# Kernel tuning notes

Measured on AMD Instinct MI355X. Metric: run time of the kernel, lower is better.

The kernel has to match this reference:

```python
import jax, jax.numpy as jnp
import numpy as np

B, T, I, H = 64, 2048, 64, 128


def setup_inputs() -> dict:
    key = jax.random.key(0)
    ks = jax.random.split(key, 6)
    std = 1.0 / np.sqrt(H)
    return {
        "x": jax.random.normal(ks[0], (B, T, I), dtype=jnp.float32),
        "h0": jax.random.normal(ks[1], (B, H), dtype=jnp.float32),
        "W": jax.random.uniform(ks[2], (H, I), dtype=jnp.float32, minval=-std, maxval=std),
        "U": jax.random.uniform(ks[3], (H, H), dtype=jnp.float32, minval=-std, maxval=std),
        "b_ih": jax.random.uniform(ks[4], (H,), dtype=jnp.float32, minval=-std, maxval=std),
        "b_hh": jax.random.uniform(ks[5], (H,), dtype=jnp.float32, minval=-std, maxval=std),
    }


def reference(x, h0, W, U, b_ih, b_hh):
    # Precompute the input projection for all timesteps in one big GEMM:
    # xw[b,t,h] = W x_t + b_ih + b_hh  (biases folded in once)
    xw = jnp.einsum("bti,hi->bth", x, W) + b_ih + b_hh  # [B,T,H]
    xw_t = jnp.swapaxes(xw, 0, 1)  # [T,B,H] for scan over time

    def step(h, xt):
        # vanilla tanh RNN cell: h' = tanh(W x + U h + b_ih + b_hh)
        h_new = jnp.tanh(xt + h @ U.T)
        return h_new, h_new

    h_last, ys = jax.lax.scan(step, h0, xw_t)  # ys: [T,B,H]
    output = jnp.swapaxes(ys, 0, 1)  # batch_first -> [B,T,H]
    return output, h_last
```

## Files before the change

kernel.cpp:

```cpp
#include <hip/hip_runtime.h>
#include <hip/hip_bf16.h>


#define RNN_B 64
#define RNN_T 2048
#define RNN_I 64
#define RNN_H 128
#define CH    32
#define NCH   (RNN_T / CH)

__device__ __forceinline__ float fast_tanh(float x) {
  float e = __builtin_amdgcn_exp2f(x * 2.885390081777927f);
  return 1.0f - 2.0f * __builtin_amdgcn_rcpf(e + 1.0f);
}

template <int CTRL>
__device__ __forceinline__ float dpp_add(float s) {
  int o = __builtin_amdgcn_mov_dpp(__float_as_int(s), CTRL, 0xF, 0xF, true);
  return s + __int_as_float(o);
}

__global__ __launch_bounds__(256) void rnn_xw_gemm(
    const float* __restrict__ x, const float* __restrict__ W,
    const float* __restrict__ b_ih, const float* __restrict__ b_hh,
    float* __restrict__ xw) {
  const int tid  = threadIdx.x;
  const int h    = tid >> 1;
  const int half = tid & 1;

  const float4* W4 = (const float4*)(W + h * RNN_I + half * 32);
  float4 w[8];
#pragma unroll
  for (int j = 0; j < 8; ++j) w[j] = W4[j];
  const float bias = b_ih[h] + b_hh[h];

  __shared__ __align__(16) float4 xs[64 * 16];
  const long rbase = (long)blockIdx.x * 64;
  const float4* xg = (const float4*)(x + rbase * RNN_I);
#pragma unroll
  for (int j = 0; j < 4; ++j) xs[tid + 256 * j] = xg[tid + 256 * j];
  __syncthreads();

  for (int r = 0; r < 64; ++r) {
    const float4* xr = xs + r * 16 + half * 8;
    float4 a = make_float4(0.f, 0.f, 0.f, 0.f);
#pragma unroll
    for (int j = 0; j < 8; ++j) {
      float4 xv = xr[j];
      a.x = fmaf(w[j].x, xv.x, a.x);
      a.y = fmaf(w[j].y, xv.y, a.y);
      a.z = fmaf(w[j].z, xv.z, a.z);
      a.w = fmaf(w[j].w, xv.w, a.w);
    }
    float s = (a.x + a.y) + (a.z + a.w);
    s = dpp_add<0xB1>(s);
    if (half == 0)
      xw[(rbase + r) * RNN_H + h] = s + bias;
  }
}

__global__ __launch_bounds__(512, 2) void rnn_scan(
    const float* xw,
    float* out, float* __restrict__ hlast,
    const float* __restrict__ h0, const float* __restrict__ U) {
  const int b   = blockIdx.x;
  const int tid = threadIdx.x;
  const int h   = tid >> 2;
  const int q   = tid & 3;

  __shared__ __align__(16) float hbuf[2][4 * 36];
  __shared__ __align__(16) float xbuf[CH * RNN_H];
  __shared__ __align__(16) float obuf[CH * RNN_H];

  const float4* U4 = (const float4*)(U + h * RNN_H + q * 32);
  float4 u[8];
#pragma unroll
  for (int j = 0; j < 8; ++j) u[j] = U4[j];

  if (tid < RNN_H) hbuf[0][(tid >> 5) * 36 + (tid & 31)] = h0[b * RNN_H + tid];

  const long base    = (long)b * RNN_T * RNN_H;
  const float4* xw4  = (const float4*)(xw + base);
  float4* out4       = (float4*)(out + base);
  float4* xb4        = (float4*)xbuf;
  const float4* ob4  = (const float4*)obuf;

  int cur = 0;
  for (int c = 0; c < NCH; ++c) {
    float4 xr0 = xw4[(long)c * 1024 + tid];
    float4 xr1 = xw4[(long)c * 1024 + tid + 512];
    if (c > 0) {
      float4 o0 = ob4[tid];
      float4 o1 = ob4[tid + 512];
      out4[(long)(c - 1) * 1024 + tid]       = o0;
      out4[(long)(c - 1) * 1024 + tid + 512] = o1;
    }
    xb4[tid]       = xr0;
    xb4[tid + 512] = xr1;
    __syncthreads();

    for (int tc = 0; tc < CH; ++tc) {
      const float4* hp = (const float4*)(hbuf[cur] + q * 36);
      float4 a = make_float4(0.f, 0.f, 0.f, 0.f);
#pragma unroll
      for (int j = 0; j < 8; ++j) {
        float4 hv = hp[j];
        a.x = fmaf(u[j].x, hv.x, a.x);
        a.y = fmaf(u[j].y, hv.y, a.y);
        a.z = fmaf(u[j].z, hv.z, a.z);
        a.w = fmaf(u[j].w, hv.w, a.w);
      }
      float s = (a.x + a.y) + (a.z + a.w);
      s = dpp_add<0xB1>(s);
      s = dpp_add<0x4E>(s);
      float val = fast_tanh(s + xbuf[tc * RNN_H + h]);
      if (q == 0) hbuf[cur ^ 1][(h >> 5) * 36 + (h & 31)] = val;
      if (q == 1) obuf[tc * RNN_H + h] = val;
      cur ^= 1;
      __syncthreads();
    }
  }

  out4[(long)(NCH - 1) * 1024 + tid]       = ob4[tid];
  out4[(long)(NCH - 1) * 1024 + tid + 512] = ob4[tid + 512];
  if (tid < RNN_H)
    hlast[b * RNN_H + tid] = hbuf[cur][(tid >> 5) * 36 + (tid & 31)];
}

extern "C" void kernel_launch(void* const* d_in, const int* in_sizes, int n_in,
                              void* d_out, int out_size, void* d_ws, size_t ws_size,
                              hipStream_t stream) {
  const float* x    = (const float*)d_in[0];
  const float* h0   = (const float*)d_in[1];
  const float* W    = (const float*)d_in[2];
  const float* U    = (const float*)d_in[3];
  const float* b_ih = (const float*)d_in[4];
  const float* b_hh = (const float*)d_in[5];

  float* out   = (float*)d_out;
  float* hlast = out + (long)RNN_B * RNN_T * RNN_H;

  rnn_xw_gemm<<<(RNN_B * RNN_T) / 64, 256, 0, stream>>>(x, W, b_ih, b_hh, out);
  rnn_scan<<<RNN_B, 512, 0, stream>>>(out, out, hlast, h0, U);
}
```

Before: 770.5 us.

## Register-tile input GEMM over shared W and force inline-asm FMAs in scan

The input-projection GEMM drops the per-thread W-in-registers layout with DPP reduction. It now stages both the x tile and all of W in padded shared memory, and each thread computes a 4x8 register tile of outputs, which raises reuse and removes the cross-lane reduction. The recurrent scan's inner dot product is rewritten with four independent accumulators issued via inline-asm v_fma_f32 after loading all h values up front. The asm is meant to stop the compiler reordering or contracting the FMAs, but it also hides them from scheduling. The scan dominates runtime and is latency-bound per step, so the GEMM change matters little overall.

```diff
diff --git a/kernel.cpp b/kernel.cpp
--- a/kernel.cpp
+++ b/kernel.cpp
@@ -20,42 +20,77 @@
   return s + __int_as_float(o);
 }
 
+#define FMA_V(acc, uu, hh) \
+  asm("v_fma_f32 %0, %1, %2, %0" : "+v"(acc) : "v"(uu), "v"(hh))
+
 __global__ __launch_bounds__(256) void rnn_xw_gemm(
     const float* __restrict__ x, const float* __restrict__ W,
     const float* __restrict__ b_ih, const float* __restrict__ b_hh,
     float* __restrict__ xw) {
-  const int tid  = threadIdx.x;
-  const int h    = tid >> 1;
-  const int half = tid & 1;
+  const int tid = threadIdx.x;
+  const int tr  = tid >> 4;
+  const int tc  = tid & 15;
 
-  const float4* W4 = (const float4*)(W + h * RNN_I + half * 32);
-  float4 w[8];
+  __shared__ __align__(16) float xs[64 * 68];
+  __shared__ __align__(16) float ws[128 * 68];
+
+  const long rbase = (long)blockIdx.x * 64;
+
+  {
+    const float4* xg = (const float4*)(x + rbase * RNN_I);
 #pragma unroll
-  for (int j = 0; j < 8; ++j) w[j] = W4[j];
-  const float bias = b_ih[h] + b_hh[h];
-
-  __shared__ __align__(16) float4 xs[64 * 16];
-  const long rbase = (long)blockIdx.x * 64;
-  const float4* xg = (const float4*)(x + rbase * RNN_I);
+    for (int j = 0; j < 4; ++j) {
+      int idx = tid + 256 * j;
+      int r = idx >> 4, k4 = idx & 15;
+      *(float4*)(&xs[r * 68 + k4 * 4]) = xg[idx];
+    }
+  }
+  {
+    const float4* wg = (const float4*)W;
 #pragma unroll
-  for (int j = 0; j < 4; ++j) xs[tid + 256 * j] = xg[tid + 256 * j];
+    for (int j = 0; j < 8; ++j) {
+      int idx = tid + 256 * j;
+      int c = idx >> 4, k4 = idx & 15;
+      *(float4*)(&ws[c * 68 + k4 * 4]) = wg[idx];
+    }
+  }
+  float bias[8];
+#pragma unroll
+  for (int cc = 0; cc < 8; ++cc)
+    bias[cc] = b_ih[tc + 16 * cc] + b_hh[tc + 16 * cc];
   __syncthreads();
 
-  for (int r = 0; r < 64; ++r) {
-    const float4* xr = xs + r * 16 + half * 8;
-    float4 a = make_float4(0.f, 0.f, 0.f, 0.f);
+  float acc[4][8];
 #pragma unroll
-    for (int j = 0; j < 8; ++j) {
-      float4 xv = xr[j];
-      a.x = fmaf(w[j].x, xv.x, a.x);
-      a.y = fmaf(w[j].y, xv.y, a.y);
-      a.z = fmaf(w[j].z, xv.z, a.z);
-      a.w = fmaf(w[j].w, xv.w, a.w);
-    }
-    float s = (a.x + a.y) + (a.z + a.w);
-    s = dpp_add<0xB1>(s);
-    if (half == 0)
-      xw[(rbase + r) * RNN_H + h] = s + bias;
+  for (int rr = 0; rr < 4; ++rr)
+#pragma unroll
+    for (int cc = 0; cc < 8; ++cc) acc[rr][cc] = 0.f;
+
+  for (int kc = 0; kc < 16; ++kc) {
+    float4 xv[4], wv[8];
+#pragma unroll
+    for (int rr = 0; rr < 4; ++rr)
+      xv[rr] = *(const float4*)(&xs[(tr + 16 * rr) * 68 + kc * 4]);
+#pragma unroll
+    for (int cc = 0; cc < 8; ++cc)
+      wv[cc] = *(const float4*)(&ws[(tc + 16 * cc) * 68 + kc * 4]);
+#pragma unroll
+    for (int rr = 0; rr < 4; ++rr)
+#pragma unroll
+      for (int cc = 0; cc < 8; ++cc) {
+        acc[rr][cc] = fmaf(xv[rr].x, wv[cc].x, acc[rr][cc]);
+        acc[rr][cc] = fmaf(xv[rr].y, wv[cc].y, acc[rr][cc]);
+        acc[rr][cc] = fmaf(xv[rr].z, wv[cc].z, acc[rr][cc]);
+        acc[rr][cc] = fmaf(xv[rr].w, wv[cc].w, acc[rr][cc]);
+      }
+  }
+
+#pragma unroll
+  for (int rr = 0; rr < 4; ++rr) {
+    long row = rbase + tr + 16 * rr;
+#pragma unroll
+    for (int cc = 0; cc < 8; ++cc)
+      xw[row * RNN_H + tc + 16 * cc] = acc[rr][cc] + bias[cc];
   }
 }
 
@@ -101,16 +136,28 @@
 
     for (int tc = 0; tc < CH; ++tc) {
       const float4* hp = (const float4*)(hbuf[cur] + q * 36);
-      float4 a = make_float4(0.f, 0.f, 0.f, 0.f);
-#pragma unroll
-      for (int j = 0; j < 8; ++j) {
-        float4 hv = hp[j];
-        a.x = fmaf(u[j].x, hv.x, a.x);
-        a.y = fmaf(u[j].y, hv.y, a.y);
-        a.z = fmaf(u[j].z, hv.z, a.z);
-        a.w = fmaf(u[j].w, hv.w, a.w);
-      }
-      float s = (a.x + a.y) + (a.z + a.w);
+      float4 h0v = hp[0], h1v = hp[1], h2v = hp[2], h3v = hp[3];
+      float4 h4v = hp[4], h5v = hp[5], h6v = hp[6], h7v = hp[7];
+
+      float a0 = 0.f, a1 = 0.f, a2 = 0.f, a3 = 0.f;
+      FMA_V(a0, u[0].x, h0v.x); FMA_V(a1, u[0].y, h0v.y);
+      FMA_V(a2, u[0].z, h0v.z); FMA_V(a3, u[0].w, h0v.w);
+      FMA_V(a0, u[1].x, h1v.x); FMA_V(a1, u[1].y, h1v.y);
+      FMA_V(a2, u[1].z, h1v.z); FMA_V(a3, u[1].w, h1v.w);
+      FMA_V(a0, u[2].x, h2v.x); FMA_V(a1, u[2].y, h2v.y);
+      FMA_V(a2, u[2].z, h2v.z); FMA_V(a3, u[2].w, h2v.w);
+      FMA_V(a0, u[3].x, h3v.x); FMA_V(a1, u[3].y, h3v.y);
+      FMA_V(a2, u[3].z, h3v.z); FMA_V(a3, u[3].w, h3v.w);
+      FMA_V(a0, u[4].x, h4v.x); FMA_V(a1, u[4].y, h4v.y);
+      FMA_V(a2, u[4].z, h4v.z); FMA_V(a3, u[4].w, h4v.w);
+      FMA_V(a0, u[5].x, h5v.x); FMA_V(a1, u[5].y, h5v.y);
+      FMA_V(a2, u[5].z, h5v.z); FMA_V(a3, u[5].w, h5v.w);
+      FMA_V(a0, u[6].x, h6v.x); FMA_V(a1, u[6].y, h6v.y);
+      FMA_V(a2, u[6].z, h6v.z); FMA_V(a3, u[6].w, h6v.w);
+      FMA_V(a0, u[7].x, h7v.x); FMA_V(a1, u[7].y, h7v.y);
+      FMA_V(a2, u[7].z, h7v.z); FMA_V(a3, u[7].w, h7v.w);
+
+      float s = (a0 + a1) + (a2 + a3);
       s = dpp_add<0xB1>(s);
       s = dpp_add<0x4E>(s);
       float val = fast_tanh(s + xbuf[tc * RNN_H + h]);
```

After: 792.9 us. 1.03x slower.
